# Kernel optimization log

Measured on AMD Instinct MI355X. Metric: run time of the kernel, lower is better.

## Reference

```python
import jax, jax.numpy as jnp
import numpy as np

B, S, N_ITEMS, E, H, L, DFF = 32, 512, 2048, 512, 8, 2, 2048
DK = E // H
EPS = 1e-5


def setup_inputs() -> dict:
    key = jax.random.key(0)
    ks = jax.random.split(key, 32)
    sc = 0.02
    p = {
        'input_seq': jax.random.normal(ks[0], (B, S, N_ITEMS), jnp.float32),
        'emb_W': jax.random.normal(ks[1], (N_ITEMS, E), jnp.float32) * sc,
        'emb_b': jnp.zeros((E,), jnp.float32),
        'pos_emb': jax.random.normal(ks[2], (S, E), jnp.float32) * sc,
        'Wq': jax.random.normal(ks[3], (L, E, E), jnp.float32) * sc,
        'bq': jnp.zeros((L, E), jnp.float32),
        'Wk': jax.random.normal(ks[4], (L, E, E), jnp.float32) * sc,
        'bk': jnp.zeros((L, E), jnp.float32),
        'Wv': jax.random.normal(ks[5], (L, E, E), jnp.float32) * sc,
        'bv': jnp.zeros((L, E), jnp.float32),
        'Wo': jax.random.normal(ks[6], (L, E, E), jnp.float32) * sc,
        'bo': jnp.zeros((L, E), jnp.float32),
        'ln1_g': jnp.ones((L, E), jnp.float32),
        'ln1_b': jnp.zeros((L, E), jnp.float32),
        'W1': jax.random.normal(ks[7], (L, E, DFF), jnp.float32) * sc,
        'b1': jnp.zeros((L, DFF), jnp.float32),
        'W2': jax.random.normal(ks[8], (L, DFF, E), jnp.float32) * sc,
        'b2': jnp.zeros((L, E), jnp.float32),
        'ln2_g': jnp.ones((L, E), jnp.float32),
        'ln2_b': jnp.zeros((L, E), jnp.float32),
        'fc_W': jax.random.normal(ks[9], (E, 1), jnp.float32) * sc,
        'fc_b': jnp.zeros((1,), jnp.float32),
    }
    return p


def _layernorm(x, g, b):
    m = jnp.mean(x, axis=-1, keepdims=True)
    v = jnp.mean(jnp.square(x - m), axis=-1, keepdims=True)
    return (x - m) * jax.lax.rsqrt(v + EPS) * g + b


def reference(input_seq, emb_W, emb_b, pos_emb, Wq, bq, Wk, bk, Wv, bv, Wo, bo,
              ln1_g, ln1_b, W1, b1, W2, b2, ln2_g, ln2_b, fc_W, fc_b):
    x = input_seq @ emb_W + emb_b          # [B,S,E]
    x = x + pos_emb[None, :, :]
    tril = jnp.tril(jnp.ones((S, S), jnp.float32))  # causal lower-triangular
    for l in range(L):
        # --- self attention (faithful: tril BEFORE scale, zeros not -inf) ---
        q = (x @ Wq[l] + bq[l]).reshape(B, S, H, DK).transpose(0, 2, 1, 3)
        k = (x @ Wk[l] + bk[l]).reshape(B, S, H, DK).transpose(0, 2, 1, 3)
        v = (x @ Wv[l] + bv[l]).reshape(B, S, H, DK).transpose(0, 2, 1, 3)
        scores = jnp.einsum('bhqd,bhkd->bhqk', q, k)
        scores = (scores * tril) / np.sqrt(DK)
        probs = jax.nn.softmax(scores, axis=-1)
        attn = jnp.einsum('bhqk,bhkd->bhqd', probs, v)  # [B,H,S,DK]
        attn = attn.transpose(0, 2, 1, 3).reshape(B, S, E)
        attn = attn @ Wo[l] + bo[l]
        # faithful source bug: `self_attention(x,x,x)[0]` -> batch 0 only,
        # broadcast over all batches in the residual add
        attended0 = attn[0]                 # [S,E]
        x = _layernorm(x + attended0[None, :, :], ln1_g[l], ln1_b[l])
        # --- feed forward ---
        ff = jax.nn.relu(x @ W1[l] + b1[l]) @ W2[l] + b2[l]
        x = _layernorm(x + ff, ln2_g[l], ln2_b[l])
    out = (x @ fc_W + fc_b).squeeze(-1)     # [B,S]
    return out
```

## Files before the change

kernel.cpp:

```cpp
#include <hip/hip_runtime.h>


typedef __bf16 bf16;
typedef __bf16 bf16x8 __attribute__((ext_vector_type(8)));
typedef __bf16 bf16x4 __attribute__((ext_vector_type(4)));
typedef float  f32x4  __attribute__((ext_vector_type(4)));

#define SEQ 512

__device__ __forceinline__ void gl2lds16(const bf16* g, void* l) {
    __builtin_amdgcn_global_load_lds(
        (const __attribute__((address_space(1))) void*)g,
        (__attribute__((address_space(3))) void*)l, 16, 0, 0);
}

template<int N> __device__ __forceinline__ void waitvm() {
    if constexpr (N == 0)      asm volatile("s_waitcnt vmcnt(0)" ::: "memory");
    else if constexpr (N == 2) asm volatile("s_waitcnt vmcnt(2)" ::: "memory");
    else if constexpr (N == 3) asm volatile("s_waitcnt vmcnt(3)" ::: "memory");
    else if constexpr (N == 4) asm volatile("s_waitcnt vmcnt(4)" ::: "memory");
    else if constexpr (N == 5) asm volatile("s_waitcnt vmcnt(5)" ::: "memory");
    else if constexpr (N == 6) asm volatile("s_waitcnt vmcnt(6)" ::: "memory");
    else if constexpr (N == 8) asm volatile("s_waitcnt vmcnt(8)" ::: "memory");
    else static_assert(N == 0, "unsupported waitvm");
}

__global__ __launch_bounds__(512, 1)
void fattn(const bf16* __restrict__ qkv,
           const bf16* __restrict__ VT,
           bf16* __restrict__ attn0b)
{
    __shared__ __align__(1024) char smem[65536 + 65536 + 8192];
    char* Ks = smem;
    char* Vs = smem + 65536;
    const int h = blockIdx.y;
    const int q0 = blockIdx.x * 128;
    const int tid = threadIdx.x, lane = tid & 63, wv = tid >> 6;
    const int fr = lane & 15, fc = lane >> 4;
    char* Ps = smem + 131072 + wv * 1024;

    {
        const bf16* Kg = qkv + 512 + h * 64;
        #pragma unroll
        for (int p = 0; p < 8; ++p) {
            int row = p * 64 + (tid >> 3);
            int ch  = tid & 7;
            gl2lds16(Kg + (long long)row * 1536 + ((ch ^ (row & 7)) * 8),
                     Ks + p * 8192 + tid * 16);
        }
        const bf16* Vg = VT + (long long)h * 64 * 512;
        #pragma unroll
        for (int p = 0; p < 8; ++p) {
            int row = p * 8 + (tid >> 6);
            int ch  = tid & 63;
            int chg = (ch & ~7) | ((ch & 7) ^ (row & 7));
            gl2lds16(Vg + (long long)row * 512 + chg * 8,
                     Vs + p * 8192 + tid * 16);
        }
    }
    const int q0w = q0 + wv * 16;
    const int qg  = q0w + fr;
    bf16x8 qf[2];
    #pragma unroll
    for (int w = 0; w < 2; ++w)
        qf[w] = *(const bf16x8*)(qkv + (long long)qg * 1536 + h * 64 + w * 32 + fc * 8);

    asm volatile("s_waitcnt vmcnt(0)" ::: "memory");
    __builtin_amdgcn_s_barrier();
    asm volatile("" ::: "memory");

    f32x4 s[32] = {};
    #pragma unroll
    for (int kt = 0; kt < 32; ++kt) {
        #pragma unroll
        for (int w = 0; w < 2; ++w) {
            int row = kt * 16 + fr;
            bf16x8 kf = *(const bf16x8*)(Ks + row * 128 +
                                         (((w * 4 + fc) ^ (row & 7)) * 16));
            s[kt] = __builtin_amdgcn_mfma_f32_16x16x32_bf16(kf, qf[w], s[kt], 0, 0, 0);
        }
    }

    float mx = -3.4e38f;
    #pragma unroll
    for (int kt = 0; kt < 32; ++kt)
        #pragma unroll
        for (int rr = 0; rr < 4; ++rr) {
            int k = kt * 16 + fc * 4 + rr;
            float v = (k <= qg) ? s[kt][rr] * 0.125f : 0.0f;
            s[kt][rr] = v;
            mx = fmaxf(mx, v);
        }
    mx = fmaxf(mx, __shfl_xor(mx, 16));
    mx = fmaxf(mx, __shfl_xor(mx, 32));
    float sum = 0.f;
    #pragma unroll
    for (int kt = 0; kt < 32; ++kt)
        #pragma unroll
        for (int rr = 0; rr < 4; ++rr) {
            float e = __expf(s[kt][rr] - mx);
            s[kt][rr] = e;
            sum += e;
        }
    sum += __shfl_xor(sum, 16);
    sum += __shfl_xor(sum, 32);
    const float inv = 1.0f / sum;

    f32x4 o[4] = {};
    #pragma unroll
    for (int kt2 = 0; kt2 < 16; ++kt2) {
        bf16x4 u0, u1;
        #pragma unroll
        for (int rr = 0; rr < 4; ++rr) {
            u0[rr] = (bf16)(s[2 * kt2][rr] * inv);
            u1[rr] = (bf16)(s[2 * kt2 + 1][rr] * inv);
        }
        *(bf16x4*)(Ps + fr * 64 + ((fc ^ (fr & 7)) * 8))       = u0;
        *(bf16x4*)(Ps + fr * 64 + (((4 + fc) ^ (fr & 7)) * 8)) = u1;
        __threadfence_block();
        bf16x4 lo = *(const bf16x4*)(Ps + fr * 64 + (((2 * fc) ^ (fr & 7)) * 8));
        bf16x4 hi = *(const bf16x4*)(Ps + fr * 64 + (((2 * fc + 1) ^ (fr & 7)) * 8));
        bf16x8 pf;
        pf[0] = lo[0]; pf[1] = lo[1]; pf[2] = lo[2]; pf[3] = lo[3];
        pf[4] = hi[0]; pf[5] = hi[1]; pf[6] = hi[2]; pf[7] = hi[3];
        #pragma unroll
        for (int n = 0; n < 4; ++n) {
            int row = n * 16 + fr;
            int ch  = kt2 * 4 + fc;
            int chs = (ch & ~7) | ((ch & 7) ^ (row & 7));
            bf16x8 vf = *(const bf16x8*)(Vs + row * 1024 + chs * 16);
            o[n] = __builtin_amdgcn_mfma_f32_16x16x32_bf16(pf, vf, o[n], 0, 0, 0);
        }
    }

    #pragma unroll
    for (int n = 0; n < 4; ++n)
        #pragma unroll
        for (int rr = 0; rr < 4; ++rr) {
            int qrow = q0w + fc * 4 + rr;
            attn0b[(long long)qrow * 512 + h * 64 + n * 16 + fr] = (bf16)o[n][rr];
        }
}

template<int BN, int ACT, int POS>
__global__ __launch_bounds__(512, 1)
void mg8(const bf16* __restrict__ Ab, int lda,
         const bf16* __restrict__ Bt, int ldb,
         const float* __restrict__ bias, const float* __restrict__ pos,
         bf16* __restrict__ Cb, int ldc, int K)
{
    constexpr int BM = 256;
    constexpr int APASS = 2;
    constexpr int BPASS = BN / 128;
    constexpr int AHB = BM * 64;
    constexpr int BHB = BN * 64;
    constexpr int WM = (BN == 256 ? 2 : 4), WN = 8 / WM;
    constexpr int MR = BM / WM / 16;
    constexpr int NR = BN / WN / 16;
    __shared__ __align__(1024) char smem[4 * AHB + 4 * BHB];
    char* ABase = smem;
    char* BBase = smem + 4 * AHB;

    const int gx = gridDim.x, gy = gridDim.y;
    const int nwg = gx * gy;
    const int b = blockIdx.y * gx + blockIdx.x;
    const int q = nwg >> 3, r = nwg & 7;
    const int xcd = b & 7, loc = b >> 3;
    const int wg = (xcd < r ? xcd * (q + 1) : r * (q + 1) + (xcd - r) * q) + loc;
    const int bx = wg % gx, by = wg / gx;
    const int row0 = by * BM, col0 = bx * BN;

    const int tid = threadIdx.x, lane = tid & 63, wv = tid >> 6;
    const int wr = (WM == 2 ? (wv >> 2) : (wv >> 1));
    const int wc = (WM == 2 ? (wv & 3) : (wv & 1));
    const int fr = lane & 15, fc = lane >> 4;

    const bf16* aS[APASS];
    #pragma unroll
    for (int p = 0; p < APASS; ++p) {
        int cL = p * 512 + tid;
        int row = cL >> 2, ch = cL & 3;
        aS[p] = Ab + (long long)(row0 + row) * lda + ((ch ^ (row & 3)) * 8);
    }
    const bf16* bS[BPASS];
    #pragma unroll
    for (int p = 0; p < BPASS; ++p) {
        int cL = p * 512 + tid;
        int row = cL >> 2, ch = cL & 3;
        bS[p] = Bt + (long long)(col0 + row) * ldb + ((ch ^ (row & 3)) * 8);
    }
    int aOff[MR], bOff[NR];
    #pragma unroll
    for (int m = 0; m < MR; ++m) {
        int row = wr * (BM / WM) + m * 16 + fr;
        aOff[m] = row * 64 + ((fc ^ (row & 3)) * 16);
    }
    #pragma unroll
    for (int n = 0; n < NR; ++n) {
        int row = wc * (BN / WN) + n * 16 + fr;
        bOff[n] = row * 64 + ((fc ^ (row & 3)) * 16);
    }

    auto stagePart = [&](int j) {
        const int tau = j >> 2, kh = (j >> 1) & 1, d = tau & 1;
        const int koff = tau * 64 + kh * 32;
        if (!(j & 1)) {
            char* dst = ABase + (d * 2 + kh) * AHB + wv * 1024;
            #pragma unroll
            for (int p = 0; p < APASS; ++p)
                gl2lds16(aS[p] + koff, dst + p * 8192);
        } else {
            char* dst = BBase + (d * 2 + kh) * BHB + wv * 1024;
            #pragma unroll
            for (int p = 0; p < BPASS; ++p)
                gl2lds16(bS[p] + koff, dst + p * 8192);
        }
    };

    const int nt = K >> 6;
    const int T = 4 * nt;
    #pragma unroll
    for (int j = 0; j < 6; ++j)
        if (j < T) stagePart(j);
    waitvm<2 * (APASS + BPASS)>();
    __builtin_amdgcn_s_barrier();

    f32x4 acc[MR][NR] = {};
    const int NPH = 2 * nt;
    for (int g = 0; g < NPH; ++g) {
        const int tau = g >> 1, ks = g & 1, d = tau & 1;

        const char* as = ABase + (d * 2 + ks) * AHB;
        const char* bs = BBase + (d * 2 + ks) * BHB;
        bf16x8 a[MR], b2[NR];
        #pragma unroll
        for (int m = 0; m < MR; ++m) a[m] = *(const bf16x8*)(as + aOff[m]);
        #pragma unroll
        for (int n = 0; n < NR; ++n) b2[n] = *(const bf16x8*)(bs + bOff[n]);

        if (2 * g + 6 < T) stagePart(2 * g + 6);
        if (2 * g + 7 < T) stagePart(2 * g + 7);

        __builtin_amdgcn_s_setprio(1);
        #pragma unroll
        for (int m = 0; m < MR; ++m)
            #pragma unroll
            for (int n = 0; n < NR; ++n)
                acc[m][n] = __builtin_amdgcn_mfma_f32_16x16x32_bf16(
                    a[m], b2[n], acc[m][n], 0, 0, 0);
        __builtin_amdgcn_s_setprio(0);

        const int rem = T - (2 * g + 4);
        if (rem >= 4)      waitvm<2 * (APASS + BPASS)>();
        else if (rem == 3) waitvm<2 * APASS + BPASS>();
        else if (rem == 2) waitvm<APASS + BPASS>();
        else if (rem == 1) waitvm<APASS>();
        else               waitvm<0>();
        __builtin_amdgcn_s_barrier();
    }

    float* st = (float*)(smem + wv * 4096);
    const int rowb = row0 + wr * (BM / WM);
    const int colb = col0 + wc * (BN / WN);
    #pragma unroll
    for (int m = 0; m < MR; ++m) {
        #pragma unroll
        for (int n = 0; n < NR; ++n) {
            int col = colb + n * 16 + fr;
            float bb = bias ? bias[col] : 0.f;
            #pragma unroll
            for (int rr = 0; rr < 4; ++rr) {
                float x = acc[m][n][rr] + bb;
                if constexpr (POS) {
                    int rowg = rowb + m * 16 + fc * 4 + rr;
                    x += pos[(rowg & 511) * 512 + col];
                }
                if constexpr (ACT) x = fmaxf(x, 0.f);
                st[(fc * 4 + rr) * 64 + n * 16 + fr] = x;
            }
        }
        #pragma unroll
        for (int sgi = 0; sgi < 2; ++sgi) {
            int row = sgi * 8 + (lane >> 3);
            int c8 = (lane & 7) * 8;
            f32x4 u = *(const f32x4*)&st[row * 64 + c8];
            f32x4 v = *(const f32x4*)&st[row * 64 + c8 + 4];
            bf16x8 w8;
            w8[0] = (bf16)u[0]; w8[1] = (bf16)u[1];
            w8[2] = (bf16)u[2]; w8[3] = (bf16)u[3];
            w8[4] = (bf16)v[0]; w8[5] = (bf16)v[1];
            w8[6] = (bf16)v[2]; w8[7] = (bf16)v[3];
            *(bf16x8*)&Cb[(long long)(rowb + m * 16 + row) * ldc + colb + c8] = w8;
        }
    }
}

template<int BM, int BN, int ACT, int CMODE, int CAUSAL>
__global__ __launch_bounds__(256, 4)
void mgemm(const bf16* __restrict__ Ab, int lda, long long sA,
           const bf16* __restrict__ Bt, int ldb, long long sB,
           const float* __restrict__ bias,
           float* __restrict__ Cf, bf16* __restrict__ Cb, int ldc, long long sC,
           int K)
{
    static_assert(BM == 128 && (BN == 128 || BN == 64), "tile");
    const int gx = gridDim.x, gy = gridDim.y;
    const int nwg = gx * gy;
    const int b = blockIdx.y * gx + blockIdx.x;
    const int q = nwg >> 3, r = nwg & 7;
    const int xcd = b & 7, loc = b >> 3;
    const int wg = (xcd < r ? xcd * (q + 1) : r * (q + 1) + (xcd - r) * q) + loc;
    const int bx = wg % gx, by = wg / gx;
    if (CAUSAL && bx * BN > by * BM + (BM - 1)) return;

    constexpr int TM = BM / 32, TN = BN / 32;
    constexpr int AIT = BM / 64, BIT = BN / 64;
    constexpr int ABY = BM * 64;
    constexpr int BBY = BN * 64;
    __shared__ bf16 As[2 * BM * 32];
    __shared__ bf16 Bs[2 * BN * 32];
    char* AsB = (char*)As;
    char* BsB = (char*)Bs;
    const int tid = threadIdx.x;
    const int lane = tid & 63, wv = tid >> 6;
    const int wr = wv >> 1, wc = wv & 1;
    const int fr = lane & 15, fc = lane >> 4;
    const int row0 = by * BM, col0 = bx * BN;
    const int z = blockIdx.z;

    Ab += (long long)z * sA;
    Bt += (long long)z * sB;
    if constexpr (CMODE == 0) Cf += (long long)z * sC;
    else                      Cb += (long long)z * sC;

    f32x4 acc[TM][TN] = {};

    const bf16* aSrc[AIT];
    #pragma unroll
    for (int it = 0; it < AIT; ++it) {
        int cL = it * 256 + tid;
        int row = cL >> 2, ch = cL & 3;
        aSrc[it] = Ab + (long long)(row0 + row) * lda + ((ch ^ (row & 3)) * 8);
    }
    const bf16* bSrc[BIT];
    #pragma unroll
    for (int it = 0; it < BIT; ++it) {
        int cL = it * 256 + tid;
        int row = cL >> 2, ch = cL & 3;
        bSrc[it] = Bt + (long long)(col0 + row) * ldb + ((ch ^ (row & 3)) * 8);
    }
    int aOff[TM], bOff[TN];
    #pragma unroll
    for (int m = 0; m < TM; ++m) {
        int row = wr * (BM / 2) + m * 16 + fr;
        aOff[m] = row * 64 + ((fc ^ (row & 3)) * 16);
    }
    #pragma unroll
    for (int n = 0; n < TN; ++n) {
        int row = wc * (BN / 2) + n * 16 + fr;
        bOff[n] = row * 64 + ((fc ^ (row & 3)) * 16);
    }

    auto stageTo = [&](int buf, int kt) {
        #pragma unroll
        for (int it = 0; it < AIT; ++it)
            gl2lds16(aSrc[it] + kt, AsB + buf * ABY + it * 4096 + wv * 1024);
        #pragma unroll
        for (int it = 0; it < BIT; ++it)
            gl2lds16(bSrc[it] + kt, BsB + buf * BBY + it * 4096 + wv * 1024);
    };

    const int nt = K >> 5;
    stageTo(0, 0);
    asm volatile("s_waitcnt vmcnt(0)" ::: "memory");
    __builtin_amdgcn_s_barrier();
    asm volatile("" ::: "memory");

    int cur = 0;
    for (int t = 0; t < nt; ++t) {
        if (t + 1 < nt) stageTo(cur ^ 1, (t + 1) * 32);
        bf16x8 a[TM], b2[TN];
        #pragma unroll
        for (int m = 0; m < TM; ++m) a[m] = *(const bf16x8*)(AsB + cur * ABY + aOff[m]);
        #pragma unroll
        for (int n = 0; n < TN; ++n) b2[n] = *(const bf16x8*)(BsB + cur * BBY + bOff[n]);
        __builtin_amdgcn_s_setprio(1);
        #pragma unroll
        for (int m = 0; m < TM; ++m)
            #pragma unroll
            for (int n = 0; n < TN; ++n)
                acc[m][n] = __builtin_amdgcn_mfma_f32_16x16x32_bf16(a[m], b2[n], acc[m][n], 0, 0, 0);
        __builtin_amdgcn_s_setprio(0);
        if (t + 1 < nt) {
            asm volatile("s_waitcnt vmcnt(0)" ::: "memory");
            __builtin_amdgcn_s_barrier();
            asm volatile("" ::: "memory");
            cur ^= 1;
        }
    }

    #pragma unroll
    for (int n = 0; n < TN; ++n) {
        int col = col0 + wc * (BN / 2) + n * 16 + fr;
        float bb = bias ? bias[col] : 0.f;
        #pragma unroll
        for (int m = 0; m < TM; ++m) {
            int rbase = row0 + wr * (BM / 2) + m * 16 + fc * 4;
            #pragma unroll
            for (int rr = 0; rr < 4; ++rr) {
                float x = acc[m][n][rr] + bb;
                if constexpr (ACT) x = fmaxf(x, 0.f);
                long long ci = (long long)(rbase + rr) * ldc + col;
                if constexpr (CMODE == 0) Cf[ci] = x;
                else                      Cb[ci] = (bf16)x;
            }
        }
    }
}

__global__ __launch_bounds__(256)
void cvt_k(const float* __restrict__ in, bf16* __restrict__ outb, long long n8)
{
    long long i = (long long)blockIdx.x * 256 + threadIdx.x;
    const long long stride = (long long)gridDim.x * 256;
    for (; i < n8; i += stride) {
        const float* p = in + i * 8;
        float4 u = *(const float4*)p;
        float4 v = *(const float4*)(p + 4);
        bf16x8 w8;
        w8[0] = (bf16)u.x; w8[1] = (bf16)u.y; w8[2] = (bf16)u.z; w8[3] = (bf16)u.w;
        w8[4] = (bf16)v.x; w8[5] = (bf16)v.y; w8[6] = (bf16)v.z; w8[7] = (bf16)v.w;
        *(bf16x8*)(outb + i * 8) = w8;
    }
}

__global__ __launch_bounds__(256)
void wt_k(const float* __restrict__ W, bf16* __restrict__ WT, int K, int N)
{
    __shared__ float t[32][33];
    int n0 = blockIdx.x * 32, k0 = blockIdx.y * 32;
    int r = threadIdx.x >> 3, c4 = (threadIdx.x & 7) * 4;
    float4 v = *(const float4*)&W[(long long)(k0 + r) * N + n0 + c4];
    t[r][c4 + 0] = v.x; t[r][c4 + 1] = v.y;
    t[r][c4 + 2] = v.z; t[r][c4 + 3] = v.w;
    __syncthreads();
    int n = threadIdx.x >> 3, kk4 = (threadIdx.x & 7) * 4;
    bf16x4 o;
    o[0] = (bf16)t[kk4 + 0][n]; o[1] = (bf16)t[kk4 + 1][n];
    o[2] = (bf16)t[kk4 + 2][n]; o[3] = (bf16)t[kk4 + 3][n];
    *(bf16x4*)&WT[(long long)(n0 + n) * K + k0 + kk4] = o;
}

__global__ __launch_bounds__(512)
void packb_k(const float* __restrict__ bq, const float* __restrict__ bk,
             const float* __restrict__ bv, float* __restrict__ dst)
{
    int l = blockIdx.x, t = threadIdx.x;
    dst[l * 1536 + t]        = bq[l * 512 + t];
    dst[l * 1536 + 512 + t]  = bk[l * 512 + t];
    dst[l * 1536 + 1024 + t] = bv[l * 512 + t];
}

__global__ __launch_bounds__(256)
void vt_k(const bf16* __restrict__ qkv, bf16* __restrict__ VT)
{
    __shared__ bf16 t[64][80];
    int h = blockIdx.y, s0 = blockIdx.x * 64;
    int r = threadIdx.x >> 2, c16 = (threadIdx.x & 3) * 16;
    const bf16* src = qkv + (long long)(s0 + r) * 1536 + 1024 + h * 64 + c16;
    *(bf16x8*)&t[r][c16]     = *(const bf16x8*)src;
    *(bf16x8*)&t[r][c16 + 8] = *(const bf16x8*)(src + 8);
    __syncthreads();
    int d = r, seg = c16;
    bf16 tmp[16];
    #pragma unroll
    for (int j = 0; j < 16; ++j) tmp[j] = t[seg + j][d];
    bf16* dst = VT + ((long long)(h * 64 + d)) * 512 + s0 + seg;
    *(bf16x8*)dst       = *(bf16x8*)&tmp[0];
    *(bf16x8*)(dst + 8) = *(bf16x8*)&tmp[8];
}

__global__ __launch_bounds__(128)
void addln_k(bf16* __restrict__ xb, const bf16* __restrict__ res,
             unsigned resMask, const float* __restrict__ g,
             const float* __restrict__ bta)
{
    long long row = blockIdx.x;
    int tid = threadIdx.x;
    int c = tid * 4;
    bf16x4 xv4 = *(const bf16x4*)&xb[row * 512 + c];
    bf16x4 rv4 = *(const bf16x4*)&res[(long long)(blockIdx.x & resMask) * 512 + c];
    float x0 = (float)xv4[0] + (float)rv4[0];
    float x1 = (float)xv4[1] + (float)rv4[1];
    float x2 = (float)xv4[2] + (float)rv4[2];
    float x3 = (float)xv4[3] + (float)rv4[3];
    float s = x0 + x1 + x2 + x3;
    float qq = x0 * x0 + x1 * x1 + x2 * x2 + x3 * x3;
    #pragma unroll
    for (int off = 32; off; off >>= 1) {
        s += __shfl_xor(s, off);
        qq += __shfl_xor(qq, off);
    }
    __shared__ float rs[2], rq[2];
    if ((tid & 63) == 0) { rs[tid >> 6] = s; rq[tid >> 6] = qq; }
    __syncthreads();
    s = rs[0] + rs[1]; qq = rq[0] + rq[1];
    float mean = s * (1.0f / 512.0f);
    float var  = qq * (1.0f / 512.0f) - mean * mean;
    float rstd = rsqrtf(var + 1e-5f);
    float4 gv = *(const float4*)&g[c];
    float4 bv = *(const float4*)&bta[c];
    bf16x4 o4;
    o4[0] = (bf16)((x0 - mean) * rstd * gv.x + bv.x);
    o4[1] = (bf16)((x1 - mean) * rstd * gv.y + bv.y);
    o4[2] = (bf16)((x2 - mean) * rstd * gv.z + bv.z);
    o4[3] = (bf16)((x3 - mean) * rstd * gv.w + bv.w);
    *(bf16x4*)&xb[row * 512 + c] = o4;
}

__global__ __launch_bounds__(256)
void fc_k(const bf16* __restrict__ x, const float* __restrict__ w,
          const float* __restrict__ bb, float* __restrict__ out)
{
    int row  = blockIdx.x * 4 + (threadIdx.x >> 6);
    int lane = threadIdx.x & 63;
    const bf16* xr = x + (long long)row * 512;
    bf16x8 a8 = *(const bf16x8*)&xr[lane * 8];
    float4 w0 = *(const float4*)&w[lane * 8];
    float4 w1 = *(const float4*)&w[lane * 8 + 4];
    float s = (float)a8[0] * w0.x + (float)a8[1] * w0.y
            + (float)a8[2] * w0.z + (float)a8[3] * w0.w
            + (float)a8[4] * w1.x + (float)a8[5] * w1.y
            + (float)a8[6] * w1.z + (float)a8[7] * w1.w;
    #pragma unroll
    for (int off = 32; off; off >>= 1) s += __shfl_xor(s, off);
    if (lane == 0) out[row] = s + bb[0];
}

extern "C" void kernel_launch(void* const* d_in, const int* in_sizes, int n_in,
                              void* d_out, int out_size, void* d_ws, size_t ws_size,
                              hipStream_t stream)
{
    const float* input_seq = (const float*)d_in[0];
    const float* emb_W  = (const float*)d_in[1];
    const float* emb_b  = (const float*)d_in[2];
    const float* pos_emb= (const float*)d_in[3];
    const float* Wq = (const float*)d_in[4];
    const float* bq = (const float*)d_in[5];
    const float* Wk = (const float*)d_in[6];
    const float* bk = (const float*)d_in[7];
    const float* Wv = (const float*)d_in[8];
    const float* bv = (const float*)d_in[9];
    const float* Wo = (const float*)d_in[10];
    const float* bo = (const float*)d_in[11];
    const float* ln1_g = (const float*)d_in[12];
    const float* ln1_b = (const float*)d_in[13];
    const float* W1 = (const float*)d_in[14];
    const float* b1 = (const float*)d_in[15];
    const float* W2 = (const float*)d_in[16];
    const float* b2 = (const float*)d_in[17];
    const float* ln2_g = (const float*)d_in[18];
    const float* ln2_b = (const float*)d_in[19];
    const float* fcW = (const float*)d_in[20];
    const float* fcb = (const float*)d_in[21];
    float* out = (float*)d_out;

    char* w = (char*)d_ws;
    size_t off = 0;
    auto alloc = [&](size_t bytes) -> void* {
        off = (off + 255) & ~(size_t)255;
        void* p = w + off;
        off += bytes;
        return p;
    };
    bf16*  xb     = (bf16*) alloc(16384ull * 512 * 2);
    bf16*  embWT  = (bf16*) alloc(512ull * 2048 * 2);
    bf16*  qkvWT  = (bf16*) alloc(2ull * 1536 * 512 * 2);
    bf16*  WoT    = (bf16*) alloc(2ull * 512 * 512 * 2);
    bf16*  W1T    = (bf16*) alloc(2ull * 2048 * 512 * 2);
    bf16*  W2T    = (bf16*) alloc(2ull * 512 * 2048 * 2);
    float* qkvB   = (float*)alloc(2ull * 1536 * 4);
    off = (off + 255) & ~(size_t)255;
    char* dynp = w + off;
    bf16*  seqb     = (bf16*)dynp;
    bf16*  qkv      = (bf16*)dynp;
    bf16*  VT       = (bf16*)(dynp + 1572864);
    bf16*  attn0b   = (bf16*)(dynp + 1572864 + 524288);
    bf16*  attnout0b= (bf16*)(dynp + 1572864 + 524288 + 524288);
    bf16*  hidden = (bf16*)dynp;
    bf16*  ffout  = (bf16*)(dynp + 16384ull * 2048 * 2);

    dim3 blk(256);
    dim3 blk512(512);

    wt_k<<<dim3(16, 64), blk, 0, stream>>>(emb_W, embWT, 2048, 512);
    for (int l = 0; l < 2; ++l) {
        wt_k<<<dim3(16, 16), blk, 0, stream>>>(Wq + l * 262144, qkvWT + l * 786432,          512, 512);
        wt_k<<<dim3(16, 16), blk, 0, stream>>>(Wk + l * 262144, qkvWT + l * 786432 + 262144, 512, 512);
        wt_k<<<dim3(16, 16), blk, 0, stream>>>(Wv + l * 262144, qkvWT + l * 786432 + 524288, 512, 512);
        wt_k<<<dim3(16, 16), blk, 0, stream>>>(Wo + l * 262144, WoT + l * 262144, 512, 512);
        wt_k<<<dim3(64, 16), blk, 0, stream>>>(W1 + l * 1048576, W1T + l * 1048576, 512, 2048);
        wt_k<<<dim3(16, 64), blk, 0, stream>>>(W2 + l * 1048576, W2T + l * 1048576, 2048, 512);
    }
    packb_k<<<dim3(2), dim3(512), 0, stream>>>(bq, bk, bv, qkvB);
    cvt_k<<<dim3(2048), blk, 0, stream>>>(input_seq, seqb, 16384ll * 2048 / 8);

    mg8<128, 0, 1><<<dim3(4, 64), blk512, 0, stream>>>(
        seqb, 2048, embWT, 2048, emb_b, pos_emb, xb, 512, 2048);

    for (int l = 0; l < 2; ++l) {
        const bf16* qkvWT_l = qkvWT + l * 786432;
        const bf16* WoT_l   = WoT + l * 262144;
        const bf16* W1T_l   = W1T + l * 1048576;
        const bf16* W2T_l   = W2T + l * 1048576;

        mgemm<128, 128, 0, 1, 0><<<dim3(12, 4), blk, 0, stream>>>(
            xb, 512, 0, qkvWT_l, 512, 0, qkvB + l * 1536,
            nullptr, qkv, 1536, 0, 512);
        vt_k<<<dim3(8, 8), blk, 0, stream>>>(qkv, VT);
        fattn<<<dim3(4, 8), blk512, 0, stream>>>(qkv, VT, attn0b);
        mgemm<128, 128, 0, 1, 0><<<dim3(4, 4), blk, 0, stream>>>(
            attn0b, 512, 0, WoT_l, 512, 0, bo + l * 512, nullptr,
            attnout0b, 512, 0, 512);
        addln_k<<<dim3(16384), dim3(128), 0, stream>>>(
            xb, attnout0b, 511u, ln1_g + l * 512, ln1_b + l * 512);

        mg8<256, 1, 0><<<dim3(8, 64), blk512, 0, stream>>>(
            xb, 512, W1T_l, 512, b1 + l * 2048, nullptr, hidden, 2048, 512);
        mg8<128, 0, 0><<<dim3(4, 64), blk512, 0, stream>>>(
            hidden, 2048, W2T_l, 2048, b2 + l * 512, nullptr, ffout, 512, 2048);
        addln_k<<<dim3(16384), dim3(128), 0, stream>>>(
            xb, ffout, 0xffffffffu, ln2_g + l * 512, ln2_b + l * 512);
    }

    fc_k<<<dim3(4096), blk, 0, stream>>>(xb, fcW, fcb, out);
}
```

Before: 402.2 us.

## Merge weight-prep launches, unroll input conversion, and shrink attention-GEMM tiles

Replaces thirteen weight-transpose launches and the bias-pack launch with a single wtall_k kernel that picks its source matrix from the block index, cutting per-launch overhead. The fp32-to-bf16 conversion of the input sequence now runs on half as many blocks, with each thread handling four strided chunks so more loads are in flight. The QKV and output-projection GEMMs, which only cover batch 0's 512 rows, switch to 128x64 tiles so twice as many workgroups run. The merged kernel adds branching per block, and the narrower tiles reuse less data per block.

```diff
diff --git a/kernel.cpp b/kernel.cpp
--- a/kernel.cpp
+++ b/kernel.cpp
@@ -23,6 +23,95 @@
     else if constexpr (N == 6) asm volatile("s_waitcnt vmcnt(6)" ::: "memory");
     else if constexpr (N == 8) asm volatile("s_waitcnt vmcnt(8)" ::: "memory");
     else static_assert(N == 0, "unsupported waitvm");
+}
+
+__global__ __launch_bounds__(256)
+void cvt_k(const float* __restrict__ in, bf16* __restrict__ outb)
+{
+    const long long gsz = (long long)gridDim.x * 256;
+    const long long n8 = 16384ll * 2048 / 8;
+    long long i = (long long)blockIdx.x * 256 + threadIdx.x;
+    for (; i + 3 * gsz < n8; i += 4 * gsz) {
+        f32x4 a0 = *(const f32x4*)(in + i * 8);
+        f32x4 b0 = *(const f32x4*)(in + i * 8 + 4);
+        f32x4 a1 = *(const f32x4*)(in + (i + gsz) * 8);
+        f32x4 b1 = *(const f32x4*)(in + (i + gsz) * 8 + 4);
+        f32x4 a2 = *(const f32x4*)(in + (i + 2 * gsz) * 8);
+        f32x4 b2 = *(const f32x4*)(in + (i + 2 * gsz) * 8 + 4);
+        f32x4 a3 = *(const f32x4*)(in + (i + 3 * gsz) * 8);
+        f32x4 b3 = *(const f32x4*)(in + (i + 3 * gsz) * 8 + 4);
+        bf16x8 w0, w1, w2, w3;
+        #pragma unroll
+        for (int j = 0; j < 4; ++j) {
+            w0[j] = (bf16)a0[j]; w0[4 + j] = (bf16)b0[j];
+            w1[j] = (bf16)a1[j]; w1[4 + j] = (bf16)b1[j];
+            w2[j] = (bf16)a2[j]; w2[4 + j] = (bf16)b2[j];
+            w3[j] = (bf16)a3[j]; w3[4 + j] = (bf16)b3[j];
+        }
+        *(bf16x8*)(outb + i * 8)             = w0;
+        *(bf16x8*)(outb + (i + gsz) * 8)     = w1;
+        *(bf16x8*)(outb + (i + 2 * gsz) * 8) = w2;
+        *(bf16x8*)(outb + (i + 3 * gsz) * 8) = w3;
+    }
+    for (; i < n8; i += gsz) {
+        f32x4 a0 = *(const f32x4*)(in + i * 8);
+        f32x4 b0 = *(const f32x4*)(in + i * 8 + 4);
+        bf16x8 w0;
+        #pragma unroll
+        for (int j = 0; j < 4; ++j) { w0[j] = (bf16)a0[j]; w0[4 + j] = (bf16)b0[j]; }
+        *(bf16x8*)(outb + i * 8) = w0;
+    }
+}
+
+__global__ __launch_bounds__(256)
+void wtall_k(const float* __restrict__ emb_W, bf16* __restrict__ embWT,
+             const float* __restrict__ Wq, const float* __restrict__ Wk,
+             const float* __restrict__ Wv, const float* __restrict__ Wo,
+             const float* __restrict__ W1, const float* __restrict__ W2,
+             bf16* __restrict__ qkvWT, bf16* __restrict__ WoT,
+             bf16* __restrict__ W1T, bf16* __restrict__ W2T,
+             const float* __restrict__ bq, const float* __restrict__ bk,
+             const float* __restrict__ bv, float* __restrict__ qkvB)
+{
+    const int b = blockIdx.x;
+    if (b < 7168) {
+        const float* src;
+        bf16* dst;
+        int K, N, t;
+        if (b < 1024) {
+            src = emb_W; dst = embWT; K = 2048; N = 512; t = b;
+        } else {
+            const int bb = b - 1024;
+            const int l = bb >= 3072 ? 1 : 0;
+            const int r = bb - l * 3072;
+            if (r < 256)       { src = Wq + l * 262144;  dst = qkvWT + l * 786432;          K = 512;  N = 512;  t = r; }
+            else if (r < 512)  { src = Wk + l * 262144;  dst = qkvWT + l * 786432 + 262144; K = 512;  N = 512;  t = r - 256; }
+            else if (r < 768)  { src = Wv + l * 262144;  dst = qkvWT + l * 786432 + 524288; K = 512;  N = 512;  t = r - 512; }
+            else if (r < 1024) { src = Wo + l * 262144;  dst = WoT + l * 262144;            K = 512;  N = 512;  t = r - 768; }
+            else if (r < 2048) { src = W1 + l * 1048576; dst = W1T + l * 1048576;           K = 512;  N = 2048; t = r - 1024; }
+            else               { src = W2 + l * 1048576; dst = W2T + l * 1048576;           K = 2048; N = 512;  t = r - 2048; }
+        }
+        const int tx = N >> 5;
+        const int n0 = (t % tx) * 32, k0 = (t / tx) * 32;
+        __shared__ float tl[32][33];
+        int r2 = threadIdx.x >> 3, c4 = (threadIdx.x & 7) * 4;
+        float4 v = *(const float4*)&src[(long long)(k0 + r2) * N + n0 + c4];
+        tl[r2][c4 + 0] = v.x; tl[r2][c4 + 1] = v.y;
+        tl[r2][c4 + 2] = v.z; tl[r2][c4 + 3] = v.w;
+        __syncthreads();
+        int n = threadIdx.x >> 3, kk4 = (threadIdx.x & 7) * 4;
+        bf16x4 o;
+        o[0] = (bf16)tl[kk4 + 0][n]; o[1] = (bf16)tl[kk4 + 1][n];
+        o[2] = (bf16)tl[kk4 + 2][n]; o[3] = (bf16)tl[kk4 + 3][n];
+        *(bf16x4*)&dst[(long long)(n0 + n) * K + k0 + kk4] = o;
+    } else {
+        const int l = b - 7168;
+        for (int t2 = threadIdx.x; t2 < 512; t2 += 256) {
+            qkvB[l * 1536 + t2]        = bq[l * 512 + t2];
+            qkvB[l * 1536 + 512 + t2]  = bk[l * 512 + t2];
+            qkvB[l * 1536 + 1024 + t2] = bv[l * 512 + t2];
+        }
+    }
 }
 
 __global__ __launch_bounds__(512, 1)
@@ -416,49 +505,6 @@
             }
         }
     }
-}
-
-__global__ __launch_bounds__(256)
-void cvt_k(const float* __restrict__ in, bf16* __restrict__ outb, long long n8)
-{
-    long long i = (long long)blockIdx.x * 256 + threadIdx.x;
-    const long long stride = (long long)gridDim.x * 256;
-    for (; i < n8; i += stride) {
-        const float* p = in + i * 8;
-        float4 u = *(const float4*)p;
-        float4 v = *(const float4*)(p + 4);
-        bf16x8 w8;
-        w8[0] = (bf16)u.x; w8[1] = (bf16)u.y; w8[2] = (bf16)u.z; w8[3] = (bf16)u.w;
-        w8[4] = (bf16)v.x; w8[5] = (bf16)v.y; w8[6] = (bf16)v.z; w8[7] = (bf16)v.w;
-        *(bf16x8*)(outb + i * 8) = w8;
-    }
-}
-
-__global__ __launch_bounds__(256)
-void wt_k(const float* __restrict__ W, bf16* __restrict__ WT, int K, int N)
-{
-    __shared__ float t[32][33];
-    int n0 = blockIdx.x * 32, k0 = blockIdx.y * 32;
-    int r = threadIdx.x >> 3, c4 = (threadIdx.x & 7) * 4;
-    float4 v = *(const float4*)&W[(long long)(k0 + r) * N + n0 + c4];
-    t[r][c4 + 0] = v.x; t[r][c4 + 1] = v.y;
-    t[r][c4 + 2] = v.z; t[r][c4 + 3] = v.w;
-    __syncthreads();
-    int n = threadIdx.x >> 3, kk4 = (threadIdx.x & 7) * 4;
-    bf16x4 o;
-    o[0] = (bf16)t[kk4 + 0][n]; o[1] = (bf16)t[kk4 + 1][n];
-    o[2] = (bf16)t[kk4 + 2][n]; o[3] = (bf16)t[kk4 + 3][n];
-    *(bf16x4*)&WT[(long long)(n0 + n) * K + k0 + kk4] = o;
-}
-
-__global__ __launch_bounds__(512)
-void packb_k(const float* __restrict__ bq, const float* __restrict__ bk,
-             const float* __restrict__ bv, float* __restrict__ dst)
-{
-    int l = blockIdx.x, t = threadIdx.x;
-    dst[l * 1536 + t]        = bq[l * 512 + t];
-    dst[l * 1536 + 512 + t]  = bk[l * 512 + t];
-    dst[l * 1536 + 1024 + t] = bv[l * 512 + t];
 }
 
 __global__ __launch_bounds__(256)
@@ -593,17 +639,10 @@
     dim3 blk(256);
     dim3 blk512(512);
 
-    wt_k<<<dim3(16, 64), blk, 0, stream>>>(emb_W, embWT, 2048, 512);
-    for (int l = 0; l < 2; ++l) {
-        wt_k<<<dim3(16, 16), blk, 0, stream>>>(Wq + l * 262144, qkvWT + l * 786432,          512, 512);
-        wt_k<<<dim3(16, 16), blk, 0, stream>>>(Wk + l * 262144, qkvWT + l * 786432 + 262144, 512, 512);
-        wt_k<<<dim3(16, 16), blk, 0, stream>>>(Wv + l * 262144, qkvWT + l * 786432 + 524288, 512, 512);
-        wt_k<<<dim3(16, 16), blk, 0, stream>>>(Wo + l * 262144, WoT + l * 262144, 512, 512);
-        wt_k<<<dim3(64, 16), blk, 0, stream>>>(W1 + l * 1048576, W1T + l * 1048576, 512, 2048);
-        wt_k<<<dim3(16, 64), blk, 0, stream>>>(W2 + l * 1048576, W2T + l * 1048576, 2048, 512);
-    }
-    packb_k<<<dim3(2), dim3(512), 0, stream>>>(bq, bk, bv, qkvB);
-    cvt_k<<<dim3(2048), blk, 0, stream>>>(input_seq, seqb, 16384ll * 2048 / 8);
+    cvt_k<<<dim3(1024), blk, 0, stream>>>(input_seq, seqb);
+    wtall_k<<<dim3(7170), blk, 0, stream>>>(
+        emb_W, embWT, Wq, Wk, Wv, Wo, W1, W2,
+        qkvWT, WoT, W1T, W2T, bq, bk, bv, qkvB);
 
     mg8<128, 0, 1><<<dim3(4, 64), blk512, 0, stream>>>(
         seqb, 2048, embWT, 2048, emb_b, pos_emb, xb, 512, 2048);
@@ -614,12 +653,12 @@
         const bf16* W1T_l   = W1T + l * 1048576;
         const bf16* W2T_l   = W2T + l * 1048576;
 
-        mgemm<128, 128, 0, 1, 0><<<dim3(12, 4), blk, 0, stream>>>(
+        mgemm<128, 64, 0, 1, 0><<<dim3(24, 4), blk, 0, stream>>>(
             xb, 512, 0, qkvWT_l, 512, 0, qkvB + l * 1536,
             nullptr, qkv, 1536, 0, 512);
         vt_k<<<dim3(8, 8), blk, 0, stream>>>(qkv, VT);
         fattn<<<dim3(4, 8), blk512, 0, stream>>>(qkv, VT, attn0b);
-        mgemm<128, 128, 0, 1, 0><<<dim3(4, 4), blk, 0, stream>>>(
+        mgemm<128, 64, 0, 1, 0><<<dim3(8, 4), blk, 0, stream>>>(
             attn0b, 512, 0, WoT_l, 512, 0, bo + l * 512, nullptr,
             attnout0b, 512, 0, 512);
         addln_k<<<dim3(16384), dim3(128), 0, stream>>>(
```

Result: faster. 366.0 us (-9.0%).
